# Kernel tuning notes

Hardware: AMD Instinct MI355X
Metric: run time of the kernel (lower is better)

Reference implementation:

```python
import jax, jax.numpy as jnp
import numpy as np

DIM = 768
HEADS = 12
DIM_HEAD = 64
INNER = HEADS * DIM_HEAD  # 768
SCALE = DIM_HEAD ** -0.5
LN_EPS = 1e-5


def setup_inputs() -> dict:
    key = jax.random.key(0)
    ks = jax.random.split(key, 6)
    B, N = 2, 1024
    x = jax.random.normal(ks[0], (B, N, DIM), dtype=jnp.float32)
    ln_g = jnp.ones((DIM,), jnp.float32)
    ln_b = jnp.zeros((DIM,), jnp.float32)
    # torch nn.Linear weights are [out, in]
    w_qkv = jax.random.normal(ks[1], (3 * INNER, DIM), jnp.float32) * (DIM ** -0.5)
    w_out = jax.random.normal(ks[2], (DIM, INNER), jnp.float32) * (INNER ** -0.5)
    b_out = jnp.zeros((DIM,), jnp.float32)
    theta = jax.random.normal(ks[3], (HEADS, HEADS), jnp.float32)
    # xavier_uniform for 12x12
    lim = float(np.sqrt(6.0 / (HEADS + HEADS)))
    gnn_w = jax.random.uniform(ks[4], (HEADS, HEADS), jnp.float32, -lim, lim)
    return {"x": x, "ln_g": ln_g, "ln_b": ln_b, "w_qkv": w_qkv,
            "w_out": w_out, "b_out": b_out, "theta": theta, "gnn_w": gnn_w}


def _dc_crd(attn, theta, gnn_w):
    # attn: [B, H, N, N] treated as image with H=12 channels
    B, H, N, _ = attn.shape
    w = attn.mean(axis=(-2, -1))  # adaptive_avg_pool2d -> [B, H]
    diff = w[:, :, None] - w[:, None, :]  # [B, H, H]
    # abs(1 - exp(-d)/(1+exp(-d))) - 1 == abs(1 - sigmoid(-d)) - 1
    T_w = jnp.abs(1.0 - jax.nn.sigmoid(-diff)) - 1.0
    adj = (T_w + jnp.swapaxes(T_w, -1, -2)) * 0.5 * theta  # [B, H, H]
    attn_flat = attn.reshape(B, H, N * N)
    support = jnp.einsum('ij,bjm->bim', gnn_w, attn_flat)  # W @ features
    out = jax.nn.relu(jnp.einsum('bij,bjm->bim', adj, support))  # spmm(adj, support)
    return out.reshape(B, H, N, N)


def reference(x, ln_g, ln_b, w_qkv, w_out, b_out, theta, gnn_w):
    B, N, D = x.shape
    mu = x.mean(-1, keepdims=True)
    var = x.var(-1, keepdims=True)
    xn = (x - mu) * jax.lax.rsqrt(var + LN_EPS) * ln_g + ln_b
    qkv = xn @ w_qkv.T  # [B, N, 3*INNER]
    q, k, v = jnp.split(qkv, 3, axis=-1)
    def heads(t):
        return t.reshape(B, N, HEADS, DIM_HEAD).transpose(0, 2, 1, 3)
    q, k, v = heads(q), heads(k), heads(v)  # [B, H, N, d]
    dots = jnp.einsum('bhnd,bhmd->bhnm', q, k) * SCALE
    attn = jax.nn.softmax(dots, axis=-1)
    H = _dc_crd(attn, theta, gnn_w)
    out = jnp.einsum('bhnm,bhmd->bhnd', attn + H, v)
    out = out.transpose(0, 2, 1, 3).reshape(B, N, INNER)
    return out @ w_out.T + b_out
```

## Files before the change

kernel.cpp:

```cpp
#include <hip/hip_runtime.h>
#include <hip/hip_bf16.h>
#include <stdint.h>

#define NB 2
#define SEQ 1024
#define DMODEL 768
#define NH 12
#define DH 64
#define SCALE 0.125f
#define NCH 4

typedef __hip_bfloat16 bf16;
typedef __attribute__((ext_vector_type(8))) short short8;
typedef __attribute__((ext_vector_type(4))) float f32x4;

__device__ __forceinline__ float b2f(bf16 x){ return __bfloat162float(x); }
__device__ __forceinline__ bf16 f2b(float x){ return __float2bfloat16(x); }
__device__ __forceinline__ short f2bs(float x){
  bf16 h = __float2bfloat16(x); return *reinterpret_cast<short*>(&h);
}

__global__ __launch_bounds__(256) void cvt_kernel(const float* __restrict__ src,
                                                  bf16* __restrict__ dst, int n){
  int i = blockIdx.x*256 + threadIdx.x;
  if (i < n) dst[i] = f2b(src[i]);
}

__global__ __launch_bounds__(256) void ln_kernel(const float* __restrict__ x,
                                                 const float* __restrict__ g,
                                                 const float* __restrict__ bta,
                                                 bf16* __restrict__ xn){
  int row = blockIdx.x; int t = threadIdx.x;
  const float* xr = x + (size_t)row*DMODEL;
  float v0[3]; float s = 0.f, s2 = 0.f;
  #pragma unroll
  for (int i=0;i<3;i++){ float val = xr[t+256*i]; v0[i]=val; s+=val; s2+=val*val; }
  __shared__ float sb[256], s2b[256];
  sb[t]=s; s2b[t]=s2; __syncthreads();
  for (int off=128; off>0; off>>=1){
    if (t<off){ sb[t]+=sb[t+off]; s2b[t]+=s2b[t+off]; }
    __syncthreads();
  }
  float mean = sb[0]*(1.f/DMODEL);
  float var  = s2b[0]*(1.f/DMODEL) - mean*mean;
  float rstd = rsqrtf(var + 1e-5f);
  #pragma unroll
  for (int i=0;i<3;i++){
    int c = t+256*i;
    xn[(size_t)row*DMODEL + c] = f2b((v0[i]-mean)*rstd*g[c] + bta[c]);
  }
}

__global__ __launch_bounds__(256) void prep_kernel(const float* __restrict__ theta,
                                                   const float* __restrict__ gnn,
                                                   float* __restrict__ Mm,
                                                   float* __restrict__ l){
  int bx = blockIdx.x, t = threadIdx.x;
  if (bx == 0){
    if (t < 144){
      int i = t/12, kx = t%12;
      float sacc = 0.f;
      for (int j=0;j<12;j++) sacc += (-0.5f)*theta[i*12+j] * gnn[j*12+kx];
      Mm[t] = sacc;
    }
  } else {
    l[(bx-1)*256 + t] = 0.f;
  }
}

__global__ __launch_bounds__(256) void gemm_qkv(const bf16* __restrict__ A,
                                                const bf16* __restrict__ W,
                                                bf16* __restrict__ q,
                                                bf16* __restrict__ k,
                                                bf16* __restrict__ vt){
  __shared__ bf16 As[128*32];
  __shared__ bf16 Bs[128*32];
  int n0 = blockIdx.x*128, m0 = blockIdx.y*128;
  int t = threadIdx.x, w = t>>6, lane = t&63;
  int ln16 = lane&15, q8 = (lane>>4)*8;
  int wm = w>>1, wn = w&1;
  f32x4 acc[4][4] = {};
  for (int k0=0; k0<768; k0+=32){
    __syncthreads();
    #pragma unroll
    for (int i=0;i<2;i++){
      int cc = t + i*256;
      int r = cc>>2, ko = (cc&3)*8;
      *(short8*)&As[r*32+ko] = *(const short8*)&A[(size_t)(m0+r)*768 + k0+ko];
      *(short8*)&Bs[r*32+ko] = *(const short8*)&W[(size_t)(n0+r)*768 + k0+ko];
    }
    __syncthreads();
    short8 af[4], bfr[4];
    #pragma unroll
    for (int mi=0;mi<4;mi++) af[mi]  = *(const short8*)&As[(wm*64+mi*16+ln16)*32 + q8];
    #pragma unroll
    for (int ni=0;ni<4;ni++) bfr[ni] = *(const short8*)&Bs[(wn*64+ni*16+ln16)*32 + q8];
    #pragma unroll
    for (int mi=0;mi<4;mi++)
      #pragma unroll
      for (int ni=0;ni<4;ni++)
        acc[mi][ni] = __builtin_amdgcn_mfma_f32_16x16x32_bf16(af[mi], bfr[ni], acc[mi][ni], 0, 0, 0);
  }
  int quad4 = (lane>>4)*4;
  #pragma unroll
  for (int mi=0;mi<4;mi++){
    #pragma unroll
    for (int ni=0;ni<4;ni++){
      int cg = n0 + wn*64 + ni*16 + ln16;
      int which = cg/768; int rem = cg - which*768;
      int h = rem>>6, dd = rem&63;
      #pragma unroll
      for (int r=0;r<4;r++){
        int m = m0 + wm*64 + mi*16 + quad4 + r;
        int bb = m>>10, n = m&1023;
        float val = acc[mi][ni][r];
        if (which==0)      q [((size_t)(bb*NH+h)*SEQ + n)*DH + dd] = f2b(val*SCALE);
        else if (which==1) k [((size_t)(bb*NH+h)*SEQ + n)*DH + dd] = f2b(val);
        else               vt[((size_t)(bb*NH+h)*DH + dd)*SEQ + n] = f2b(val);
      }
    }
  }
}

__global__ __launch_bounds__(768) void attn_sums(const bf16* __restrict__ q,
                                                 const bf16* __restrict__ k,
                                                 float* __restrict__ l){
  int b = blockIdx.z, ch = blockIdx.y; int r0 = blockIdx.x*16;
  int t = threadIdx.x; int h = t>>6; int lane = t&63;
  int ln16 = lane&15, quad = lane>>4; int q8 = quad*8, quad4 = quad*4;
  const bf16* qrow = q + ((size_t)(b*NH+h)*SEQ + r0 + ln16)*DH;
  short8 aq0 = *(const short8*)(qrow + q8);
  short8 aq1 = *(const short8*)(qrow + 32 + q8);
  const bf16* kB = k + ((size_t)(b*NH+h)*SEQ)*DH;
  float ls[4] = {0.f,0.f,0.f,0.f};
  for (int i=0;i<16;i++){
    int c0 = ch*256 + i*16;
    const bf16* krow = kB + (size_t)(c0 + ln16)*DH;
    short8 bk0 = *(const short8*)(krow + q8);
    short8 bk1 = *(const short8*)(krow + 32 + q8);
    f32x4 a = {0.f,0.f,0.f,0.f};
    a = __builtin_amdgcn_mfma_f32_16x16x32_bf16(aq0, bk0, a, 0, 0, 0);
    a = __builtin_amdgcn_mfma_f32_16x16x32_bf16(aq1, bk1, a, 0, 0, 0);
    #pragma unroll
    for (int r=0;r<4;r++) ls[r] += __expf(a[r]);
  }
  #pragma unroll
  for (int msk=1; msk<16; msk<<=1){
    #pragma unroll
    for (int r=0;r<4;r++) ls[r] += __shfl_xor(ls[r], msk);
  }
  if (ln16 == 0){
    #pragma unroll
    for (int r=0;r<4;r++)
      atomicAdd(&l[((size_t)(b*NH+h))*SEQ + r0 + quad4 + r], ls[r]);
  }
}

__global__ __launch_bounds__(768) void attn_main(const bf16* __restrict__ q,
                                                 const bf16* __restrict__ k,
                                                 const bf16* __restrict__ vt,
                                                 const float* __restrict__ Mm,
                                                 const float* __restrict__ l,
                                                 float* __restrict__ opart){
  __shared__ bf16 attT[512*16];
  __shared__ bf16 comb[12*16*40];
  int b = blockIdx.z, ch = blockIdx.y; int r0 = blockIdx.x*16;
  int t = threadIdx.x; int h = t>>6; int lane = t&63;
  int ln16 = lane&15, quad = lane>>4; int q8 = quad*8, quad4 = quad*4;
  const bf16* kB = k  + ((size_t)(b*NH+h)*SEQ)*DH;
  const bf16* vB = vt + ((size_t)(b*NH+h)*DH)*SEQ;

  if (t < 512){
    attT[t*16+12] = f2b(0.f); attT[t*16+13] = f2b(0.f);
    attT[t*16+14] = f2b(0.f); attT[t*16+15] = f2b(0.f);
  }

  short8 amix;
  #pragma unroll
  for (int j=0;j<8;j++){
    int kk = q8 + j;
    amix[j] = (ln16 < 12 && kk < 12) ? f2bs(Mm[ln16*12 + kk]) : (short)0;
  }

  const bf16* qrow = q + ((size_t)(b*NH+h)*SEQ + r0 + ln16)*DH;
  short8 aq0 = *(const short8*)(qrow + q8);
  short8 aq1 = *(const short8*)(qrow + 32 + q8);

  float inv_l[4];
  #pragma unroll
  for (int r=0;r<4;r++) inv_l[r] = 1.0f / l[((size_t)(b*NH+h))*SEQ + r0 + quad4 + r];

  f32x4 oacc[4] = {};
  for (int it=0; it<8; it++){
    int c0 = ch*256 + it*32;
    #pragma unroll
    for (int half=0; half<2; half++){
      int cc = c0 + half*16;
      const bf16* krow = kB + (size_t)(cc + ln16)*DH;
      short8 bk0 = *(const short8*)(krow + q8);
      short8 bk1 = *(const short8*)(krow + 32 + q8);
      f32x4 a = {0.f,0.f,0.f,0.f};
      a = __builtin_amdgcn_mfma_f32_16x16x32_bf16(aq0, bk0, a, 0, 0, 0);
      a = __builtin_amdgcn_mfma_f32_16x16x32_bf16(aq1, bk1, a, 0, 0, 0);
      #pragma unroll
      for (int r=0;r<4;r++){
        int pos = (quad4+r)*32 + half*16 + ln16;
        attT[pos*16 + h] = f2b(__expf(a[r])*inv_l[r]);
      }
    }
    __syncthreads();
    for (int tile=h; tile<32; tile+=12){
      short8 bfr = {0,0,0,0,0,0,0,0};
      if (quad < 2) bfr = *(const short8*)&attT[(tile*16 + ln16)*16 + q8];
      f32x4 d = {0.f,0.f,0.f,0.f};
      d = __builtin_amdgcn_mfma_f32_16x16x32_bf16(amix, bfr, d, 0, 0, 0);
      if (quad < 3){
        #pragma unroll
        for (int rr=0; rr<4; rr++){
          int hh = quad4 + rr;
          int pos = tile*16 + ln16;
          float av = b2f(attT[pos*16 + hh]);
          int r = pos>>5, c = pos&31;
          comb[(hh*16 + r)*40 + c] = f2b(av + fmaxf(d[rr], 0.f));
        }
      }
    }
    __syncthreads();
    short8 af = *(const short8*)&comb[(h*16 + ln16)*40 + q8];
    #pragma unroll
    for (int ni=0; ni<4; ni++){
      short8 bv = *(const short8*)&vB[(size_t)(ni*16 + ln16)*SEQ + c0 + q8];
      oacc[ni] = __builtin_amdgcn_mfma_f32_16x16x32_bf16(af, bv, oacc[ni], 0, 0, 0);
    }
  }
  float* dst = opart + ((size_t)ch*NB*SEQ + (size_t)b*SEQ)*DMODEL;
  #pragma unroll
  for (int ni=0; ni<4; ni++)
    #pragma unroll
    for (int r=0; r<4; r++){
      int n = r0 + quad4 + r;
      dst[(size_t)n*DMODEL + h*DH + ni*16 + ln16] = oacc[ni][r];
    }
}

__global__ __launch_bounds__(256) void reduce_kernel(const float* __restrict__ opart,
                                                     bf16* __restrict__ aout){
  const size_t TOT = (size_t)NB*SEQ*DMODEL;
  size_t i = ((size_t)blockIdx.x*256 + threadIdx.x)*4;
  float4 s = *(const float4*)&opart[i];
  #pragma unroll
  for (int c=1;c<NCH;c++){
    float4 p = *(const float4*)&opart[c*TOT + i];
    s.x += p.x; s.y += p.y; s.z += p.z; s.w += p.w;
  }
  aout[i+0]=f2b(s.x); aout[i+1]=f2b(s.y); aout[i+2]=f2b(s.z); aout[i+3]=f2b(s.w);
}

__global__ __launch_bounds__(256) void gemm_out(const bf16* __restrict__ A,
                                                const bf16* __restrict__ W,
                                                const float* __restrict__ bias,
                                                float* __restrict__ out){
  __shared__ bf16 As[128*32];
  __shared__ bf16 Bs[128*32];
  int n0 = blockIdx.x*128, m0 = blockIdx.y*128;
  int t = threadIdx.x, w = t>>6, lane = t&63;
  int ln16 = lane&15, q8 = (lane>>4)*8;
  int wm = w>>1, wn = w&1;
  f32x4 acc[4][4] = {};
  for (int k0=0; k0<768; k0+=32){
    __syncthreads();
    #pragma unroll
    for (int i=0;i<2;i++){
      int cc = t + i*256;
      int r = cc>>2, ko = (cc&3)*8;
      *(short8*)&As[r*32+ko] = *(const short8*)&A[(size_t)(m0+r)*768 + k0+ko];
      *(short8*)&Bs[r*32+ko] = *(const short8*)&W[(size_t)(n0+r)*768 + k0+ko];
    }
    __syncthreads();
    short8 af[4], bfr[4];
    #pragma unroll
    for (int mi=0;mi<4;mi++) af[mi]  = *(const short8*)&As[(wm*64+mi*16+ln16)*32 + q8];
    #pragma unroll
    for (int ni=0;ni<4;ni++) bfr[ni] = *(const short8*)&Bs[(wn*64+ni*16+ln16)*32 + q8];
    #pragma unroll
    for (int mi=0;mi<4;mi++)
      #pragma unroll
      for (int ni=0;ni<4;ni++)
        acc[mi][ni] = __builtin_amdgcn_mfma_f32_16x16x32_bf16(af[mi], bfr[ni], acc[mi][ni], 0, 0, 0);
  }
  int quad4 = (lane>>4)*4;
  #pragma unroll
  for (int mi=0;mi<4;mi++)
    #pragma unroll
    for (int ni=0;ni<4;ni++){
      int cg = n0 + wn*64 + ni*16 + ln16;
      #pragma unroll
      for (int r=0;r<4;r++){
        int m = m0 + wm*64 + mi*16 + quad4 + r;
        out[(size_t)m*768 + cg] = acc[mi][ni][r] + bias[cg];
      }
    }
}

extern "C" void kernel_launch(void* const* d_in, const int* in_sizes, int n_in,
                              void* d_out, int out_size, void* d_ws, size_t ws_size,
                              hipStream_t stream){
  const float* x     = (const float*)d_in[0];
  const float* ln_g  = (const float*)d_in[1];
  const float* ln_b  = (const float*)d_in[2];
  const float* w_qkv = (const float*)d_in[3];
  const float* w_out = (const float*)d_in[4];
  const float* b_out = (const float*)d_in[5];
  const float* theta = (const float*)d_in[6];
  const float* gnn   = (const float*)d_in[7];
  float* out = (float*)d_out;

  char* p = (char*)d_ws;
  bf16* xnb   = (bf16*)p; p += (size_t)2048*768*2;
  bf16* wqkvb = (bf16*)p; p += (size_t)2304*768*2;
  bf16* woutb = (bf16*)p; p += (size_t)768*768*2;
  bf16* qb    = (bf16*)p; p += (size_t)NB*NH*SEQ*DH*2;
  bf16* kb    = (bf16*)p; p += (size_t)NB*NH*SEQ*DH*2;
  bf16* vtb   = (bf16*)p; p += (size_t)NB*NH*SEQ*DH*2;
  bf16* aoutb = (bf16*)p; p += (size_t)2048*768*2;
  float* Mm   = (float*)p; p += 256*4;
  float* lsum = (float*)p; p += (size_t)NB*NH*SEQ*4;
  float* opart= (float*)p;

  cvt_kernel<<<dim3((2304*768+255)/256), dim3(256), 0, stream>>>(w_qkv, wqkvb, 2304*768);
  cvt_kernel<<<dim3((768*768+255)/256),  dim3(256), 0, stream>>>(w_out, woutb, 768*768);
  ln_kernel<<<dim3(NB*SEQ), dim3(256), 0, stream>>>(x, ln_g, ln_b, xnb);
  prep_kernel<<<dim3(97), dim3(256), 0, stream>>>(theta, gnn, Mm, lsum);
  gemm_qkv<<<dim3(18, 16), dim3(256), 0, stream>>>(xnb, wqkvb, qb, kb, vtb);
  attn_sums<<<dim3(64, NCH, NB), dim3(768), 0, stream>>>(qb, kb, lsum);
  attn_main<<<dim3(64, NCH, NB), dim3(768), 0, stream>>>(qb, kb, vtb, Mm, lsum, opart);
  reduce_kernel<<<dim3((NB*SEQ*DMODEL/4+255)/256), dim3(256), 0, stream>>>(opart, aoutb);
  gemm_out<<<dim3(6, 16), dim3(256), 0, stream>>>(aoutb, woutb, b_out, out);
}
```

Before: 220.4 us.

## Replace MFMA head-mixing with per-lane FMA and double-buffered LDS, one barrier

The 12x12 head-mixing step in attn_main is rewritten. Each wave now reads all 12 heads' attention probabilities for its own fragment from LDS and forms the mixed value with scalar FMAs, instead of running a padded 16x16x32 MFMA with a second LDS staging buffer. The attention buffer is double-buffered across iterations, which drops one __syncthreads per iteration and the comb array. In exchange each lane does 96 FMAs and 12 LDS vector reads per iteration, and the launch bound now asks for 6 waves per EU, which may constrain registers.

Measured after the change: 486.0 us. 2.21x slower.

```diff
diff --git a/kernel.cpp b/kernel.cpp
--- a/kernel.cpp
+++ b/kernel.cpp
@@ -18,6 +18,9 @@
 __device__ __forceinline__ bf16 f2b(float x){ return __float2bfloat16(x); }
 __device__ __forceinline__ short f2bs(float x){
   bf16 h = __float2bfloat16(x); return *reinterpret_cast<short*>(&h);
+}
+__device__ __forceinline__ float s2f(short u){
+  return __uint_as_float(((unsigned)(unsigned short)u) << 16);
 }
 
 __global__ __launch_bounds__(256) void cvt_kernel(const float* __restrict__ src,
@@ -156,31 +159,22 @@
   }
 }
 
-__global__ __launch_bounds__(768) void attn_main(const bf16* __restrict__ q,
-                                                 const bf16* __restrict__ k,
-                                                 const bf16* __restrict__ vt,
-                                                 const float* __restrict__ Mm,
-                                                 const float* __restrict__ l,
-                                                 float* __restrict__ opart){
-  __shared__ bf16 attT[512*16];
-  __shared__ bf16 comb[12*16*40];
+__global__ __launch_bounds__(768, 6) void attn_main(const bf16* __restrict__ q,
+                                                    const bf16* __restrict__ k,
+                                                    const bf16* __restrict__ vt,
+                                                    const float* __restrict__ Mm,
+                                                    const float* __restrict__ l,
+                                                    float* __restrict__ opart){
+  __shared__ bf16 attT[2][NH][16][40];
   int b = blockIdx.z, ch = blockIdx.y; int r0 = blockIdx.x*16;
   int t = threadIdx.x; int h = t>>6; int lane = t&63;
   int ln16 = lane&15, quad = lane>>4; int q8 = quad*8, quad4 = quad*4;
   const bf16* kB = k  + ((size_t)(b*NH+h)*SEQ)*DH;
   const bf16* vB = vt + ((size_t)(b*NH+h)*DH)*SEQ;
 
-  if (t < 512){
-    attT[t*16+12] = f2b(0.f); attT[t*16+13] = f2b(0.f);
-    attT[t*16+14] = f2b(0.f); attT[t*16+15] = f2b(0.f);
-  }
-
-  short8 amix;
-  #pragma unroll
-  for (int j=0;j<8;j++){
-    int kk = q8 + j;
-    amix[j] = (ln16 < 12 && kk < 12) ? f2bs(Mm[ln16*12 + kk]) : (short)0;
-  }
+  float Mrow[12];
+  #pragma unroll
+  for (int j=0;j<12;j++) Mrow[j] = Mm[h*12+j];
 
   const bf16* qrow = q + ((size_t)(b*NH+h)*SEQ + r0 + ln16)*DH;
   short8 aq0 = *(const short8*)(qrow + q8);
@@ -193,44 +187,41 @@
   f32x4 oacc[4] = {};
   for (int it=0; it<8; it++){
     int c0 = ch*256 + it*32;
+    int buf = it&1;
     #pragma unroll
     for (int half=0; half<2; half++){
-      int cc = c0 + half*16;
-      const bf16* krow = kB + (size_t)(cc + ln16)*DH;
+      const bf16* krow = kB + (size_t)(c0 + half*16 + ln16)*DH;
       short8 bk0 = *(const short8*)(krow + q8);
       short8 bk1 = *(const short8*)(krow + 32 + q8);
       f32x4 a = {0.f,0.f,0.f,0.f};
       a = __builtin_amdgcn_mfma_f32_16x16x32_bf16(aq0, bk0, a, 0, 0, 0);
       a = __builtin_amdgcn_mfma_f32_16x16x32_bf16(aq1, bk1, a, 0, 0, 0);
       #pragma unroll
-      for (int r=0;r<4;r++){
-        int pos = (quad4+r)*32 + half*16 + ln16;
-        attT[pos*16 + h] = f2b(__expf(a[r])*inv_l[r]);
-      }
-    }
-    __syncthreads();
-    for (int tile=h; tile<32; tile+=12){
-      short8 bfr = {0,0,0,0,0,0,0,0};
-      if (quad < 2) bfr = *(const short8*)&attT[(tile*16 + ln16)*16 + q8];
-      f32x4 d = {0.f,0.f,0.f,0.f};
-      d = __builtin_amdgcn_mfma_f32_16x16x32_bf16(amix, bfr, d, 0, 0, 0);
-      if (quad < 3){
-        #pragma unroll
-        for (int rr=0; rr<4; rr++){
-          int hh = quad4 + rr;
-          int pos = tile*16 + ln16;
-          float av = b2f(attT[pos*16 + hh]);
-          int r = pos>>5, c = pos&31;
-          comb[(hh*16 + r)*40 + c] = f2b(av + fmaxf(d[rr], 0.f));
-        }
-      }
-    }
-    __syncthreads();
-    short8 af = *(const short8*)&comb[(h*16 + ln16)*40 + q8];
+      for (int r=0;r<4;r++)
+        attT[buf][h][quad4+r][half*16 + ln16] = f2b(__expf(a[r])*inv_l[r]);
+    }
+    __syncthreads();
+    float s0=0.f,s1=0.f,s2=0.f,s3=0.f,s4=0.f,s5=0.f,s6=0.f,s7=0.f;
+    float a0=0.f,a1=0.f,a2=0.f,a3=0.f,a4=0.f,a5=0.f,a6=0.f,a7=0.f;
+    #pragma unroll
+    for (int j=0;j<12;j++){
+      short8 u = *(const short8*)&attT[buf][j][ln16][q8];
+      float m = Mrow[j];
+      float v0=s2f(u[0]), v1=s2f(u[1]), v2=s2f(u[2]), v3=s2f(u[3]);
+      float v4=s2f(u[4]), v5=s2f(u[5]), v6=s2f(u[6]), v7=s2f(u[7]);
+      s0 += m*v0; s1 += m*v1; s2 += m*v2; s3 += m*v3;
+      s4 += m*v4; s5 += m*v5; s6 += m*v6; s7 += m*v7;
+      if (j == h){ a0=v0; a1=v1; a2=v2; a3=v3; a4=v4; a5=v5; a6=v6; a7=v7; }
+    }
+    short8 afrag;
+    afrag[0]=f2bs(a0+fmaxf(s0,0.f)); afrag[1]=f2bs(a1+fmaxf(s1,0.f));
+    afrag[2]=f2bs(a2+fmaxf(s2,0.f)); afrag[3]=f2bs(a3+fmaxf(s3,0.f));
+    afrag[4]=f2bs(a4+fmaxf(s4,0.f)); afrag[5]=f2bs(a5+fmaxf(s5,0.f));
+    afrag[6]=f2bs(a6+fmaxf(s6,0.f)); afrag[7]=f2bs(a7+fmaxf(s7,0.f));
     #pragma unroll
     for (int ni=0; ni<4; ni++){
       short8 bv = *(const short8*)&vB[(size_t)(ni*16 + ln16)*SEQ + c0 + q8];
-      oacc[ni] = __builtin_amdgcn_mfma_f32_16x16x32_bf16(af, bv, oacc[ni], 0, 0, 0);
+      oacc[ni] = __builtin_amdgcn_mfma_f32_16x16x32_bf16(afrag, bv, oacc[ni], 0, 0, 0);
     }
   }
   float* dst = opart + ((size_t)ch*NB*SEQ + (size_t)b*SEQ)*DMODEL;
```
